# Kernel optimization log

Measured on AMD Instinct MI355X. Metric: run time of the kernel, lower is better.

The kernel has to match this reference:

```python
import jax, jax.numpy as jnp
import numpy as np

B, T, D_IN, D_H, D_CODE, N_CODES, D_OUT = 64, 512, 1024, 512, 256, 128, 100


def setup_inputs() -> dict:
    key = jax.random.key(0)
    ks = jax.random.split(key, 8)
    x = jax.random.normal(ks[0], (B, T, D_IN), dtype=jnp.float32)
    W1 = jax.random.normal(ks[1], (D_IN, D_H), dtype=jnp.float32) * (1.0 / np.sqrt(D_IN))
    b1 = jnp.zeros((D_H,), jnp.float32)
    W2 = jax.random.normal(ks[2], (D_H, D_CODE), dtype=jnp.float32) * (1.0 / np.sqrt(D_H))
    b2 = jnp.zeros((D_CODE,), jnp.float32)
    codebook = jax.random.normal(ks[3], (N_CODES, D_CODE), dtype=jnp.float32)
    Wd = jax.random.normal(ks[4], (D_CODE, D_OUT), dtype=jnp.float32) * (1.0 / np.sqrt(D_CODE))
    bd = jnp.zeros((D_OUT,), jnp.float32)
    return {"x": x, "W1": W1, "b1": b1, "W2": W2, "b2": b2,
            "codebook": codebook, "Wd": Wd, "bd": bd}


def reference(x, W1, b1, W2, b2, codebook, Wd, bd):
    Bb, Tt, _ = x.shape
    # Encoder (per-timestep loop in torch == one batched matmul)
    h = jax.nn.relu(jnp.einsum('btd,dh->bth', x, W1) + b1)
    encoded = jnp.einsum('bth,hc->btc', h, W2) + b2          # [B,T,256]
    flat = encoded.reshape(-1, D_CODE)                        # [B*T,256]
    # Squared euclidean distances (argmin identical to cdist argmin)
    d2 = (jnp.sum(flat * flat, axis=1, keepdims=True)
          - 2.0 * flat @ codebook.T
          + jnp.sum(codebook * codebook, axis=1))             # [B*T,128]
    token_indices = jnp.argmin(d2, axis=-1)                   # [B*T]
    quantized = codebook[token_indices].reshape(Bb, Tt, D_CODE)
    commitment_loss = jnp.mean((encoded - jax.lax.stop_gradient(quantized)) ** 2)
    codebook_loss = jnp.mean((quantized - jax.lax.stop_gradient(encoded)) ** 2)
    # decoded is computed in the torch model but never returned (dead code)
    pooled = encoded.mean(axis=1)
    decoded = pooled @ Wd + bd  # noqa: F841 (pruned by XLA, kept for fidelity)
    total_loss = commitment_loss + 0.25 * codebook_loss
    return (token_indices.reshape(Bb, Tt), commitment_loss, codebook_loss, total_loss)
```

## Files before the change

kernel.cpp:

```cpp
#include <hip/hip_runtime.h>
#include <cstddef>
#include <cstdint>

static constexpr int M_ROWS  = 32768;
static constexpr int D_INK   = 1024;
static constexpr int D_HID   = 512;
static constexpr int D_CODE_ = 256;
static constexpr int N_CODES_= 128;

static constexpr float TAU_GAP = 0.20f;

using f16x8 = __attribute__((ext_vector_type(8))) _Float16;
using f32x4 = __attribute__((ext_vector_type(4))) float;


__device__ __forceinline__ void dma16(const void* g, void* l) {
    __builtin_amdgcn_global_load_lds(
        (const __attribute__((address_space(1))) void*)g,
        (__attribute__((address_space(3))) void*)l, 16, 0, 0);
}

__device__ __forceinline__ void stage_panel(const _Float16* __restrict__ p,
                                            _Float16* dst, int w, int lane)
{
    #pragma unroll
    for (int ii = 0; ii < 2; ++ii) {
        const int I = 2 * w + ii;
        dma16(p + (size_t)I * 512 + lane * 8, dst + (size_t)I * 512);
    }
}

__device__ __forceinline__ void mfma_tile(const _Float16* sA, const _Float16* sB,
                                          int wm, int wn, int kq, int lm,
                                          f32x4 (&acc)[4][4])
{
    f16x8 a[4];
    #pragma unroll
    for (int fm = 0; fm < 4; ++fm)
        a[fm] = *(const f16x8*)(sA + (kq * 128 + wm * 64 + fm * 16 + lm) * 8);
    #pragma unroll
    for (int fn = 0; fn < 4; ++fn) {
        const f16x8 b = *(const f16x8*)(sB + (kq * 128 + wn * 64 + fn * 16 + lm) * 8);
        #pragma unroll
        for (int fm = 0; fm < 4; ++fm)
            acc[fm][fn] = __builtin_amdgcn_mfma_f32_16x16x32_f16(a[fm], b, acc[fm][fn], 0, 0, 0);
    }
}

__device__ __forceinline__ int xcd_swz(int bid, int nwg) {
    const int q = nwg >> 3;
    return (bid & 7) * q + (bid >> 3);
}

__global__ __launch_bounds__(256)
void prep_cb_kernel(const float* __restrict__ cb, _Float16* __restrict__ cbP,
                    float* __restrict__ cbT,
                    float* __restrict__ cbnorm, float* __restrict__ accum,
                    int* __restrict__ cnt)
{
    const int j = blockIdx.x;
    const int t = threadIdx.x;
    const float v = cb[j * D_CODE_ + t];
    const int ks = t >> 5, kq = (t >> 3) & 3, jj = t & 7;
    cbP[((size_t)ks * 512 + kq * 128 + j) * 8 + jj] = (_Float16)v;
    cbT[(size_t)t * N_CODES_ + j] = v;

    __shared__ float sr[256];
    sr[t] = v * v;
    __syncthreads();
    for (int s = 128; s >= 1; s >>= 1) {
        if (t < s) sr[t] += sr[t + s];
        __syncthreads();
    }
    if (t == 0) cbnorm[j] = sr[0];
    if (j == 0 && t < 2) accum[t] = 0.0f;
    if (j == 0 && t == 2) *cnt = 0;
}

__global__ __launch_bounds__(256)
void pack_w_kernel(const float* __restrict__ W, _Float16* __restrict__ WP,
                   int Kd, int Nd)
{
    const int ks = blockIdx.x, nt = blockIdx.y;
    const int t = threadIdx.x;
    _Float16* dst = WP + ((size_t)nt * (Kd >> 5) + ks) * 4096;
    #pragma unroll
    for (int half = 0; half < 2; ++half) {
        const int f = half * 256 + t;
        const int nc = f & 127, kq = f >> 7;
        f16x8 v;
        #pragma unroll
        for (int j = 0; j < 8; ++j)
            v[j] = (_Float16)W[(size_t)(ks * 32 + kq * 8 + j) * Nd + nt * 128 + nc];
        *(f16x8*)(dst + (size_t)f * 8) = v;
    }
}

__global__ __launch_bounds__(256)
void pack_x_kernel(const float* __restrict__ X, _Float16* __restrict__ XP)
{
    __shared__ _Float16 sh[128][136];
    const int t  = threadIdx.x;
    const int mt = blockIdx.x;
    const int kc = blockIdx.y;

    const float* src = X + (size_t)mt * 128 * D_INK + kc * 128;
    #pragma unroll
    for (int i = 0; i < 16; ++i) {
        const int idx = i * 256 + t;
        const int row = idx >> 5, c4 = idx & 31;
        const float4 v = *(const float4*)(src + (size_t)row * D_INK + c4 * 4);
        _Float16* d = &sh[row][c4 * 4];
        d[0] = (_Float16)v.x; d[1] = (_Float16)v.y;
        d[2] = (_Float16)v.z; d[3] = (_Float16)v.w;
    }
    __syncthreads();

    _Float16* dst = XP + ((size_t)mt * 32 + kc * 4) * 4096;
    #pragma unroll
    for (int s = 0; s < 4; ++s) {
        #pragma unroll
        for (int half = 0; half < 2; ++half) {
            const int f = half * 256 + t;
            const int rc = f & 127, kq = f >> 7;
            const f16x8 v = *(const f16x8*)(&sh[rc][s * 32 + kq * 8]);
            *(f16x8*)(dst + (size_t)s * 4096 + (size_t)f * 8) = v;
        }
    }
}

__global__ __launch_bounds__(256, 4)
void gemm1_kernel(const _Float16* __restrict__ AP, const _Float16* __restrict__ BP,
                  const float* __restrict__ bias, _Float16* __restrict__ CP)
{
    __shared__ _Float16 lds[2][2][4096];

    const int tid  = threadIdx.x;
    const int lane = tid & 63;
    const int w    = tid >> 6;
    const int wm = w >> 1, wn = w & 1;
    const int kq = lane >> 4, lm = lane & 15;

    const int swz = xcd_swz(blockIdx.x, (M_ROWS / 128) * (D_HID / 128));
    const int n0 = (swz & 3) * 128;
    const int m0 = (swz >> 2) * 128;

    const _Float16* Apan = AP + ((size_t)(m0 >> 7) * 32) * 4096;
    const _Float16* Bpan = BP + ((size_t)(n0 >> 7) * 32) * 4096;

    f32x4 acc[4][4] = {};

    stage_panel(Apan, &lds[0][0][0], w, lane);
    stage_panel(Bpan, &lds[0][1][0], w, lane);

    constexpr int NSTEP = D_INK / 32;
    for (int t = 0; t < NSTEP; ++t) {
        const int cur = t & 1, nxt = cur ^ 1;
        __syncthreads();
        if (t + 1 < NSTEP) {
            stage_panel(Apan + (size_t)(t + 1) * 4096, &lds[nxt][0][0], w, lane);
            stage_panel(Bpan + (size_t)(t + 1) * 4096, &lds[nxt][1][0], w, lane);
        }
        mfma_tile(&lds[cur][0][0], &lds[cur][1][0], wm, wn, kq, lm, acc);
    }

    #pragma unroll
    for (int fn = 0; fn < 4; ++fn) {
        const int col = n0 + wn * 64 + fn * 16 + lm;
        const float bv = bias[col];
        #pragma unroll
        for (int fm = 0; fm < 4; ++fm) {
            #pragma unroll
            for (int r = 0; r < 4; ++r) {
                const int row = m0 + wm * 64 + fm * 16 + kq * 4 + r;
                const float v = fmaxf(acc[fm][fn][r] + bv, 0.0f);
                CP[(((size_t)(row >> 7) * 16 + (col >> 5)) * 512
                    + (size_t)((col >> 3) & 3) * 128 + (row & 127)) * 8 + (col & 7)]
                    = (_Float16)v;
            }
        }
    }
}

__global__ __launch_bounds__(256, 4)
void gemm2_kernel(const _Float16* __restrict__ AP, const _Float16* __restrict__ BP,
                  const float* __restrict__ bias, _Float16* __restrict__ CP,
                  float* __restrict__ accum)
{
    __shared__ _Float16 lds[2][2][4096];

    const int tid  = threadIdx.x;
    const int lane = tid & 63;
    const int w    = tid >> 6;
    const int wm = w >> 1, wn = w & 1;
    const int kq = lane >> 4, lm = lane & 15;

    const int swz = xcd_swz(blockIdx.x, (M_ROWS / 128) * (D_CODE_ / 128));
    const int n0 = (swz & 1) * 128;
    const int m0 = (swz >> 1) * 128;

    const _Float16* Apan = AP + ((size_t)(m0 >> 7) * 16) * 4096;
    const _Float16* Bpan = BP + ((size_t)(n0 >> 7) * 16) * 4096;

    f32x4 acc[4][4] = {};

    stage_panel(Apan, &lds[0][0][0], w, lane);
    stage_panel(Bpan, &lds[0][1][0], w, lane);

    constexpr int NSTEP = D_HID / 32;
    for (int t = 0; t < NSTEP; ++t) {
        const int cur = t & 1, nxt = cur ^ 1;
        __syncthreads();
        if (t + 1 < NSTEP) {
            stage_panel(Apan + (size_t)(t + 1) * 4096, &lds[nxt][0][0], w, lane);
            stage_panel(Bpan + (size_t)(t + 1) * 4096, &lds[nxt][1][0], w, lane);
        }
        mfma_tile(&lds[cur][0][0], &lds[cur][1][0], wm, wn, kq, lm, acc);
    }

    float sumsq = 0.0f;
    #pragma unroll
    for (int fn = 0; fn < 4; ++fn) {
        const int col = n0 + wn * 64 + fn * 16 + lm;
        const float bv = bias[col];
        #pragma unroll
        for (int fm = 0; fm < 4; ++fm) {
            #pragma unroll
            for (int r = 0; r < 4; ++r) {
                const int row = m0 + wm * 64 + fm * 16 + kq * 4 + r;
                const float v = acc[fm][fn][r] + bv;
                sumsq = fmaf(v, v, sumsq);
                CP[(((size_t)(row >> 7) * 8 + (col >> 5)) * 512
                    + (size_t)((col >> 3) & 3) * 128 + (row & 127)) * 8 + (col & 7)]
                    = (_Float16)v;
            }
        }
    }
    #pragma unroll
    for (int mk = 1; mk <= 32; mk <<= 1) sumsq += __shfl_xor(sumsq, mk);
    if (lane == 0) atomicAdd(&accum[1], sumsq);
}

__global__ __launch_bounds__(256, 4)
void dist_kernel(const _Float16* __restrict__ AP, const _Float16* __restrict__ BP,
                 const float* __restrict__ cbn,
                 float* __restrict__ outIdx, float* __restrict__ accum,
                 int* __restrict__ cnt, int* __restrict__ list)
{
    __shared__ _Float16 lds[2][2][4096];

    const int tid  = threadIdx.x;
    const int lane = tid & 63;
    const int w    = tid >> 6;
    const int wm = w >> 1, wn = w & 1;
    const int kq = lane >> 4, lm = lane & 15;
    const int m0 = blockIdx.x * 128;

    float cbn_l[4];
    #pragma unroll
    for (int fn = 0; fn < 4; ++fn) cbn_l[fn] = cbn[wn * 64 + fn * 16 + lm];

    const _Float16* Apan = AP + ((size_t)(m0 >> 7) * 8) * 4096;

    f32x4 acc[4][4] = {};

    stage_panel(Apan, &lds[0][0][0], w, lane);
    stage_panel(BP,   &lds[0][1][0], w, lane);

    constexpr int NSTEP = D_CODE_ / 32;
    for (int t = 0; t < NSTEP; ++t) {
        const int cur = t & 1, nxt = cur ^ 1;
        __syncthreads();
        if (t + 1 < NSTEP) {
            stage_panel(Apan + (size_t)(t + 1) * 4096, &lds[nxt][0][0], w, lane);
            stage_panel(BP   + (size_t)(t + 1) * 4096, &lds[nxt][1][0], w, lane);
        }
        mfma_tile(&lds[cur][0][0], &lds[cur][1][0], wm, wn, kq, lm, acc);
    }

    __syncthreads();
    float* eb1 = (float*)&lds[0][0][0];
    float* eb2 = eb1 + 256;
    int*   eix = (int*)(eb2 + 256);

    #pragma unroll
    for (int fm = 0; fm < 4; ++fm) {
        #pragma unroll
        for (int r = 0; r < 4; ++r) {
            float b1v = 3.4e38f, b2v = 3.4e38f; int bi = 0;
            #pragma unroll
            for (int fn = 0; fn < 4; ++fn) {
                const float v = fmaf(-2.0f, acc[fm][fn][r], cbn_l[fn]);
                if (v < b1v) { b2v = b1v; b1v = v; bi = wn * 64 + fn * 16 + lm; }
                else if (v < b2v) b2v = v;
            }
            #pragma unroll
            for (int mk = 1; mk <= 8; mk <<= 1) {
                const float o1 = __shfl_xor(b1v, mk);
                const float o2 = __shfl_xor(b2v, mk);
                const int   oi = __shfl_xor(bi,  mk);
                if (o1 < b1v || (o1 == b1v && oi < bi)) { b2v = fminf(b1v, o2); b1v = o1; bi = oi; }
                else b2v = fminf(b2v, o1);
            }
            const int rl = wm * 64 + fm * 16 + kq * 4 + r;
            if (lm == 0) { eb1[wn * 128 + rl] = b1v; eb2[wn * 128 + rl] = b2v; eix[wn * 128 + rl] = bi; }
        }
    }
    __syncthreads();

    if (tid < 128) {
        const int rl = tid;
        const float a1 = eb1[rl], a2 = eb2[rl]; const int ai = eix[rl];
        const float o1 = eb1[128 + rl], o2 = eb2[128 + rl]; const int oi = eix[128 + rl];
        float B1, B2; int BI;
        if (o1 < a1 || (o1 == a1 && oi < ai)) { B1 = o1; BI = oi; B2 = fminf(a1, o2); }
        else                                  { B1 = a1; BI = ai; B2 = fminf(a2, o1); }
        outIdx[m0 + rl] = (float)BI;
        if (B2 - B1 < TAU_GAP) { const int p = atomicAdd(cnt, 1); list[p] = m0 + rl; }
        float s = B1;
        #pragma unroll
        for (int mk = 1; mk <= 32; mk <<= 1) s += __shfl_xor(s, mk);
        if (lane == 0) atomicAdd(&accum[0], s);
    }
}

__global__ __launch_bounds__(256)
void fixup_kernel(const float* __restrict__ x, const float* __restrict__ W1,
                  const float* __restrict__ b1, const float* __restrict__ W2,
                  const float* __restrict__ b2, const float* __restrict__ cbT,
                  const float* __restrict__ cbnorm,
                  const int* __restrict__ cnt, const int* __restrict__ list,
                  float* __restrict__ outIdx)
{
    __shared__ float xr[8][1024];
    __shared__ float hr[8][512];
    __shared__ float er[8][256];
    __shared__ float dv[8][128];
    __shared__ int   di[8][128];

    const int tid = threadIdx.x;
    const int n = *cnt;
    const int ngroups = (n + 7) >> 3;

    for (int g = blockIdx.x; g < ngroups; g += gridDim.x) {
        const int base = g * 8;
        const int nr = n - base < 8 ? n - base : 8;
        __syncthreads();
        #pragma unroll
        for (int r = 0; r < 8; ++r) {
            if (r < nr) {
                const int row = list[base + r];
                *(float4*)&xr[r][tid * 4] =
                    *(const float4*)(x + (size_t)row * D_INK + tid * 4);
            }
        }
        __syncthreads();

        {
            const int c = tid * 2;
            float a0[8], a1[8];
            #pragma unroll
            for (int r = 0; r < 8; ++r) { a0[r] = 0.f; a1[r] = 0.f; }
            for (int k = 0; k < D_INK; ++k) {
                const float2 wv = *(const float2*)(W1 + (size_t)k * D_HID + c);
                #pragma unroll
                for (int r = 0; r < 8; ++r) {
                    const float xv = xr[r][k];
                    a0[r] = fmaf(xv, wv.x, a0[r]);
                    a1[r] = fmaf(xv, wv.y, a1[r]);
                }
            }
            #pragma unroll
            for (int r = 0; r < 8; ++r) {
                hr[r][c]     = fmaxf(a0[r] + b1[c], 0.f);
                hr[r][c + 1] = fmaxf(a1[r] + b1[c + 1], 0.f);
            }
        }
        __syncthreads();

        {
            float a[8];
            #pragma unroll
            for (int r = 0; r < 8; ++r) a[r] = 0.f;
            for (int k = 0; k < D_HID; ++k) {
                const float wv = W2[(size_t)k * D_CODE_ + tid];
                #pragma unroll
                for (int r = 0; r < 8; ++r)
                    a[r] = fmaf(hr[r][k], wv, a[r]);
            }
            #pragma unroll
            for (int r = 0; r < 8; ++r)
                er[r][tid] = a[r] + b2[tid];
        }
        __syncthreads();

        {
            const int j = tid & 127, half = tid >> 7;
            float e2[4], dt[4];
            #pragma unroll
            for (int q = 0; q < 4; ++q) { e2[q] = 0.f; dt[q] = 0.f; }
            for (int k = 0; k < D_CODE_; ++k) {
                const float cv = cbT[(size_t)k * N_CODES_ + j];
                #pragma unroll
                for (int q = 0; q < 4; ++q) {
                    const float ev = er[half * 4 + q][k];
                    e2[q] = fmaf(ev, ev, e2[q]);
                    dt[q] = fmaf(ev, cv, dt[q]);
                }
            }
            #pragma unroll
            for (int q = 0; q < 4; ++q) {
                dv[half * 4 + q][j] = (e2[q] - 2.0f * dt[q]) + cbnorm[j];
                di[half * 4 + q][j] = j;
            }
        }
        __syncthreads();

        #pragma unroll
        for (int pass = 0; pass < 2; ++pass) {
            const int r = pass * 4 + (tid >> 6);
            const int i = tid & 63;
            {
                const float a = dv[r][i], b = dv[r][i + 64];
                const int  ib = di[r][i + 64];
                if (b < a) { dv[r][i] = b; di[r][i] = ib; }
            }
            __syncthreads();
            for (int st = 32; st >= 1; st >>= 1) {
                if (i < st) {
                    const float a = dv[r][i], b = dv[r][i + st];
                    const int  ib = di[r][i + st];
                    if (b < a || (b == a && ib < di[r][i])) { dv[r][i] = b; di[r][i] = ib; }
                }
                __syncthreads();
            }
        }
        if (tid < nr) outIdx[list[base + tid]] = (float)di[tid][0];
    }
}

__global__ void finalize_kernel(const float* __restrict__ accum, float* __restrict__ out)
{
    const float inv = 1.0f / (32768.0f * 256.0f);
    const float loss = (accum[0] + accum[1]) * inv;
    out[32768] = loss;
    out[32769] = loss;
    out[32770] = 1.25f * loss;
}

extern "C" void kernel_launch(void* const* d_in, const int* in_sizes, int n_in,
                              void* d_out, int out_size, void* d_ws, size_t ws_size,
                              hipStream_t stream)
{
    (void)in_sizes; (void)n_in; (void)out_size; (void)ws_size;

    const float* x  = (const float*)d_in[0];
    const float* W1 = (const float*)d_in[1];
    const float* b1 = (const float*)d_in[2];
    const float* W2 = (const float*)d_in[3];
    const float* b2 = (const float*)d_in[4];
    const float* cb = (const float*)d_in[5];
    float* out = (float*)d_out;

    char* ws = (char*)d_ws;
    _Float16* W1P  = (_Float16*)(ws + 0);
    _Float16* W2P  = (_Float16*)(ws + 1048576);
    _Float16* cbP  = (_Float16*)(ws + 1310720);
    float*    cbn  = (float*   )(ws + 1376256);
    float*    accum= (float*   )(ws + 1376768);
    int*      cnt  = (int*     )(ws + 1376832);
    int*      list = (int*     )(ws + 1376896);
    float*    cbT  = (float*   )(ws + 1507968);
    _Float16* xP   = (_Float16*)(ws + (size_t)(2u<<20));
    _Float16* encP = (_Float16*)(ws + (size_t)(2u<<20));
    _Float16* hP   = (_Float16*)(ws + (size_t)(2u<<20) + 67108864);

    prep_cb_kernel<<<N_CODES_, 256, 0, stream>>>(cb, cbP, cbT, cbn, accum, cnt);
    pack_w_kernel<<<dim3(D_INK / 32, D_HID / 128), 256, 0, stream>>>(W1, W1P, D_INK, D_HID);
    pack_w_kernel<<<dim3(D_HID / 32, D_CODE_ / 128), 256, 0, stream>>>(W2, W2P, D_HID, D_CODE_);
    pack_x_kernel<<<dim3(M_ROWS / 128, D_INK / 128), 256, 0, stream>>>(x, xP);

    gemm1_kernel<<<(M_ROWS / 128) * (D_HID / 128), 256, 0, stream>>>(xP, W1P, b1, hP);
    gemm2_kernel<<<(M_ROWS / 128) * (D_CODE_ / 128), 256, 0, stream>>>(hP, W2P, b2, encP, accum);
    dist_kernel<<<M_ROWS / 128, 256, 0, stream>>>(encP, cbP, cbn, out, accum, cnt, list);
    fixup_kernel<<<256, 256, 0, stream>>>(x, W1, b1, W2, b2, cbT, cbn, cnt, list, out);
    finalize_kernel<<<1, 1, 0, stream>>>(accum, out);
}
```

Before: 268.6 us.

## Broadcast fixup operands via readlane, lower gap threshold, double fixup grid

```diff
diff --git a/kernel.cpp b/kernel.cpp
--- a/kernel.cpp
+++ b/kernel.cpp
@@ -8,10 +8,14 @@
 static constexpr int D_CODE_ = 256;
 static constexpr int N_CODES_= 128;
 
-static constexpr float TAU_GAP = 0.20f;
+static constexpr float TAU_GAP = 0.15f;
 
 using f16x8 = __attribute__((ext_vector_type(8))) _Float16;
 using f32x4 = __attribute__((ext_vector_type(4))) float;
+
+__device__ __forceinline__ float rdlane(float v, int kk) {
+    return __uint_as_float(__builtin_amdgcn_readlane(__float_as_uint(v), kk));
+}
 
 
 __device__ __forceinline__ void dma16(const void* g, void* l) {
@@ -338,7 +342,8 @@
     __shared__ float dv[8][128];
     __shared__ int   di[8][128];
 
-    const int tid = threadIdx.x;
+    const int tid  = threadIdx.x;
+    const int lane = tid & 63;
     const int n = *cnt;
     const int ngroups = (n + 7) >> 3;
 
@@ -361,13 +366,19 @@
             float a0[8], a1[8];
             #pragma unroll
             for (int r = 0; r < 8; ++r) { a0[r] = 0.f; a1[r] = 0.f; }
-            for (int k = 0; k < D_INK; ++k) {
-                const float2 wv = *(const float2*)(W1 + (size_t)k * D_HID + c);
+            for (int k0 = 0; k0 < D_INK; k0 += 64) {
+                float xreg[8];
                 #pragma unroll
-                for (int r = 0; r < 8; ++r) {
-                    const float xv = xr[r][k];
-                    a0[r] = fmaf(xv, wv.x, a0[r]);
-                    a1[r] = fmaf(xv, wv.y, a1[r]);
+                for (int r = 0; r < 8; ++r) xreg[r] = xr[r][k0 + lane];
+                #pragma unroll 8
+                for (int kk = 0; kk < 64; ++kk) {
+                    const float2 wv = *(const float2*)(W1 + (size_t)(k0 + kk) * D_HID + c);
+                    #pragma unroll
+                    for (int r = 0; r < 8; ++r) {
+                        const float xv = rdlane(xreg[r], kk);
+                        a0[r] = fmaf(xv, wv.x, a0[r]);
+                        a1[r] = fmaf(xv, wv.y, a1[r]);
+                    }
                 }
             }
             #pragma unroll
@@ -382,11 +393,17 @@
             float a[8];
             #pragma unroll
             for (int r = 0; r < 8; ++r) a[r] = 0.f;
-            for (int k = 0; k < D_HID; ++k) {
-                const float wv = W2[(size_t)k * D_CODE_ + tid];
+            for (int k0 = 0; k0 < D_HID; k0 += 64) {
+                float hreg[8];
                 #pragma unroll
-                for (int r = 0; r < 8; ++r)
-                    a[r] = fmaf(hr[r][k], wv, a[r]);
+                for (int r = 0; r < 8; ++r) hreg[r] = hr[r][k0 + lane];
+                #pragma unroll 8
+                for (int kk = 0; kk < 64; ++kk) {
+                    const float wv = W2[(size_t)(k0 + kk) * D_CODE_ + tid];
+                    #pragma unroll
+                    for (int r = 0; r < 8; ++r)
+                        a[r] = fmaf(rdlane(hreg[r], kk), wv, a[r]);
+                }
             }
             #pragma unroll
             for (int r = 0; r < 8; ++r)
@@ -399,13 +416,19 @@
             float e2[4], dt[4];
             #pragma unroll
             for (int q = 0; q < 4; ++q) { e2[q] = 0.f; dt[q] = 0.f; }
-            for (int k = 0; k < D_CODE_; ++k) {
-                const float cv = cbT[(size_t)k * N_CODES_ + j];
+            for (int k0 = 0; k0 < D_CODE_; k0 += 64) {
+                float ereg[4];
                 #pragma unroll
-                for (int q = 0; q < 4; ++q) {
-                    const float ev = er[half * 4 + q][k];
-                    e2[q] = fmaf(ev, ev, e2[q]);
-                    dt[q] = fmaf(ev, cv, dt[q]);
+                for (int q = 0; q < 4; ++q) ereg[q] = er[half * 4 + q][k0 + lane];
+                #pragma unroll 8
+                for (int kk = 0; kk < 64; ++kk) {
+                    const float cv = cbT[(size_t)(k0 + kk) * N_CODES_ + j];
+                    #pragma unroll
+                    for (int q = 0; q < 4; ++q) {
+                        const float ev = rdlane(ereg[q], kk);
+                        e2[q] = fmaf(ev, ev, e2[q]);
+                        dt[q] = fmaf(ev, cv, dt[q]);
+                    }
                 }
             }
             #pragma unroll
@@ -483,6 +506,6 @@
     gemm1_kernel<<<(M_ROWS / 128) * (D_HID / 128), 256, 0, stream>>>(xP, W1P, b1, hP);
     gemm2_kernel<<<(M_ROWS / 128) * (D_CODE_ / 128), 256, 0, stream>>>(hP, W2P, b2, encP, accum);
     dist_kernel<<<M_ROWS / 128, 256, 0, stream>>>(encP, cbP, cbn, out, accum, cnt, list);
-    fixup_kernel<<<256, 256, 0, stream>>>(x, W1, b1, W2, b2, cbT, cbn, cnt, list, out);
+    fixup_kernel<<<512, 256, 0, stream>>>(x, W1, b1, W2, b2, cbT, cbn, cnt, list, out);
     finalize_kernel<<<1, 1, 0, stream>>>(accum, out);
 }
```

New measurement: 253.2 us. 5.7% less time.
